# Kernel tuning notes

Measured on AMD Instinct MI355X. Metric: run time of the kernel, lower is better.

Reference implementation:

```python
import jax, jax.numpy as jnp
import numpy as np

N_USER = 100000
N_ITEM = 200000
N_NODES = N_USER + N_ITEM
NNZ = 4000000
EMB = 64
N_LAYERS = 3
BATCH = 4096


def setup_inputs() -> dict:
    key = jax.random.key(0)
    ks = jax.random.split(key, 12)
    inp = {
        'users': jax.random.randint(ks[0], (BATCH,), 0, N_USER, dtype=jnp.int32),
        'pos_items': jax.random.randint(ks[1], (BATCH,), 0, N_ITEM, dtype=jnp.int32),
        'neg_items': jax.random.randint(ks[2], (BATCH,), 0, N_ITEM, dtype=jnp.int32),
        'row': jax.random.randint(ks[3], (NNZ,), 0, N_NODES, dtype=jnp.int32),
        'col': jax.random.randint(ks[4], (NNZ,), 0, N_NODES, dtype=jnp.int32),
        'vals': jax.random.uniform(ks[5], (NNZ,), dtype=jnp.float32),
        'user_emb': 0.1 * jax.random.normal(ks[6], (N_USER, EMB), dtype=jnp.float32),
        'item_emb': 0.1 * jax.random.normal(ks[7], (N_ITEM, EMB), dtype=jnp.float32),
        'W_gc': 0.1 * jax.random.normal(ks[8], (N_LAYERS, EMB, EMB), dtype=jnp.float32),
        'b_gc': 0.1 * jax.random.normal(ks[9], (N_LAYERS, EMB), dtype=jnp.float32),
        'W_bi': 0.1 * jax.random.normal(ks[10], (N_LAYERS, EMB, EMB), dtype=jnp.float32),
        'b_bi': 0.1 * jax.random.normal(ks[11], (N_LAYERS, EMB), dtype=jnp.float32),
    }
    return inp


def _l2_normalize(x, eps=1e-12):
    # matches torch F.normalize(p=2, dim=1): x / max(||x||, eps)
    n = jnp.sqrt(jnp.sum(x * x, axis=1, keepdims=True))
    return x / jnp.maximum(n, eps)


def reference(users, pos_items, neg_items, row, col, vals, user_emb, item_emb, W_gc, b_gc, W_bi, b_bi):
    B = users.shape[0]
    # sparse adjacency propagation: side = A_hat @ [user_emb; item_emb]
    emb = jnp.concatenate([user_emb, item_emb], axis=0)          # [N, d]
    msgs = vals[:, None] * emb[col]                               # [nnz, d]
    side = jax.ops.segment_sum(msgs, row, num_segments=N_NODES)  # [N, d]

    u_side = side[users]                                          # [B, d]
    i_side = jnp.concatenate([side[N_USER + pos_items], side[N_USER + neg_items]], axis=0)
    small_side = jnp.concatenate([u_side, i_side], axis=0)        # [3B, d]
    ego = jnp.concatenate([user_emb[users], item_emb[pos_items], item_emb[neg_items]], axis=0)

    all_embeddings = [ego]
    for k in range(N_LAYERS):
        sum_e = small_side @ W_gc[k] + b_gc[k]
        bi = (ego * small_side) @ W_bi[k] + b_bi[k]
        ego = jax.nn.leaky_relu(sum_e + bi, negative_slope=0.2)
        all_embeddings.append(_l2_normalize(ego))

    all_e = jnp.concatenate(all_embeddings, axis=1)               # [3B, d*(L+1)]
    u_g = all_e[:B]
    i_g = all_e[B:]
    pos_g = i_g[:B]
    neg_g = i_g[B:]
    return (u_g, pos_g, neg_g)
```

## Files before the change

### kernel.cpp

```cpp
#include <hip/hip_runtime.h>

#define N_USER   100000
#define N_ITEM   200000
#define N_NODES  300000
#define NNZ      4000000
#define EMB      64
#define N_LAYERS 3
#define BATCH    4096
#define NSLOT    (3*BATCH)
#define MAXE     96
#define HCAP     256
#define BMWORDS  9376


#define CNT4   3072
#define BM4    2344

__global__ void __launch_bounds__(256) k_clear(int4* __restrict__ c4,
                                               int4* __restrict__ b4) {
    int i = blockIdx.x * blockDim.x + threadIdx.x;
    if (i < CNT4)            c4[i] = make_int4(0, 0, 0, 0);
    else if (i < CNT4 + BM4) b4[i - CNT4] = make_int4(0, 0, 0, 0);
}

__global__ void k_setup(const int* __restrict__ users,
                        const int* __restrict__ pos,
                        const int* __restrict__ neg,
                        unsigned short* __restrict__ table16,
                        unsigned int* __restrict__ bitmap) {
    int i = blockIdx.x * blockDim.x + threadIdx.x;
    if (i >= NSLOT) return;
    int node;
    if (i < BATCH)            node = users[i];
    else if (i < 2 * BATCH)   node = N_USER + pos[i - BATCH];
    else                      node = N_USER + neg[i - 2 * BATCH];
    table16[node] = (unsigned short)i;
    atomicOr(&bitmap[((unsigned)node) >> 5], 1u << (node & 31));
}

__global__ void __launch_bounds__(256) k_build(
        const int* __restrict__ row,
        const int* __restrict__ col,
        const float* __restrict__ vals,
        const unsigned int* __restrict__ bitmap,
        const unsigned short* __restrict__ table16,
        int* __restrict__ count,
        int2* __restrict__ csr2) {
    __shared__ int   ls_s[HCAP];
    __shared__ int   ls_c[HCAP];
    __shared__ float ls_v[HCAP];
    __shared__ int   cnt;
    int tid = threadIdx.x;
    if (tid == 0) cnt = 0;
    __syncthreads();

    int t = blockIdx.x * 256 + tid;
    if (t < NNZ / 4) {
        int4   r = ((const int4*)row)[t];
        int4   c = ((const int4*)col)[t];
        float4 v = ((const float4*)vals)[t];
        bool h0 = (bitmap[((unsigned)r.x) >> 5] >> (r.x & 31)) & 1;
        bool h1 = (bitmap[((unsigned)r.y) >> 5] >> (r.y & 31)) & 1;
        bool h2 = (bitmap[((unsigned)r.z) >> 5] >> (r.z & 31)) & 1;
        bool h3 = (bitmap[((unsigned)r.w) >> 5] >> (r.w & 31)) & 1;
        int rr[4] = { r.x, r.y, r.z, r.w };
        int cc[4] = { c.x, c.y, c.z, c.w };
        float vv[4] = { v.x, v.y, v.z, v.w };
        bool hh[4] = { h0, h1, h2, h3 };
        #pragma unroll
        for (int i = 0; i < 4; ++i) {
            if (hh[i]) {
                int si = (int)table16[rr[i]];
                int p = atomicAdd(&cnt, 1);
                if (p < HCAP) { ls_s[p] = si; ls_c[p] = cc[i]; ls_v[p] = vv[i]; }
                else {
                    int pp = atomicAdd(&count[si], 1);
                    if (pp < MAXE)
                        csr2[(size_t)si * MAXE + pp] = make_int2(cc[i], __float_as_int(vv[i]));
                }
            }
        }
    }
    __syncthreads();

    int n = cnt; n = (n < HCAP) ? n : HCAP;
    for (int t2 = tid; t2 < n; t2 += 256) {
        int si = ls_s[t2];
        int p = atomicAdd(&count[si], 1);
        if (p < MAXE)
            csr2[(size_t)si * MAXE + p] = make_int2(ls_c[t2], __float_as_int(ls_v[t2]));
    }
}

__global__ void __launch_bounds__(256) k_gather(
        const int* __restrict__ users,
        const int* __restrict__ pos,
        const int* __restrict__ neg,
        const float* __restrict__ user_emb,
        const float* __restrict__ item_emb,
        const unsigned short* __restrict__ table16,
        const int* __restrict__ count,
        const int2* __restrict__ csr2,
        float* __restrict__ side) {
    int tid = threadIdx.x;
    int w = tid >> 6;
    int j = tid & 63;
    int slot = blockIdx.x * 4 + w;

    int node;
    if (slot < BATCH)          node = users[slot];
    else if (slot < 2 * BATCH) node = N_USER + pos[slot - BATCH];
    else                       node = N_USER + neg[slot - 2 * BATCH];

    int wslot = (int)table16[node];
    wslot = __builtin_amdgcn_readfirstlane(wslot);
    int n = count[wslot];
    n = (n < MAXE) ? n : MAXE;
    n = __builtin_amdgcn_readfirstlane(n);
    const int2* base = csr2 + (size_t)wslot * MAXE;

    float acc = 0.f;
    for (int t0 = 0; t0 < n; t0 += 64) {
        int idx = t0 + j;
        int2 ev = make_int2(0, 0);
        if (idx < n) ev = base[idx];
        int m = n - t0; m = (m < 64) ? m : 64;
        for (int tt = 0; tt < m; tt += 16) {
            float vv[16], gg[16];
            #pragma unroll
            for (int k = 0; k < 16; ++k) {
                int  t  = tt + k;
                bool okk = t < m;
                int   cc = __shfl(ev.x, t, 64);
                float vb = __uint_as_float((unsigned)__shfl(ev.y, t, 64));
                vv[k] = okk ? vb : 0.f;
                int ci = okk ? cc : 0;
                const float* sp = (ci < N_USER) ? (user_emb + (size_t)ci * EMB)
                                                : (item_emb + (size_t)(ci - N_USER) * EMB);
                gg[k] = sp[j];
            }
            #pragma unroll
            for (int k = 0; k < 16; ++k) acc = fmaf(vv[k], gg[k], acc);
        }
    }
    side[(size_t)slot * EMB + j] = acc;
}

__global__ void __launch_bounds__(256) k_mlp(
        const int* __restrict__ users,
        const int* __restrict__ pos,
        const int* __restrict__ neg,
        const float* __restrict__ user_emb,
        const float* __restrict__ item_emb,
        const float* __restrict__ W_gc,
        const float* __restrict__ b_gc,
        const float* __restrict__ W_bi,
        const float* __restrict__ b_bi,
        const float* __restrict__ side,
        float* __restrict__ out) {
    __shared__ float wg[EMB * EMB];
    __shared__ float wb[EMB * EMB];
    int tid = threadIdx.x;
    int w = tid >> 6;
    int j = tid & 63;
    int sbase = blockIdx.x * 16 + w * 4;

    float sval[4], e[4];
    #pragma unroll
    for (int s = 0; s < 4; ++s) {
        int slot = sbase + s;
        int node;
        if (slot < BATCH)          node = users[slot];
        else if (slot < 2 * BATCH) node = N_USER + pos[slot - BATCH];
        else                       node = N_USER + neg[slot - 2 * BATCH];
        const float* erow = (node < N_USER) ? (user_emb + (size_t)node * EMB)
                                            : (item_emb + (size_t)(node - N_USER) * EMB);
        e[s]    = erow[j];
        sval[s] = side[(size_t)slot * EMB + j];
        out[(size_t)slot * 256 + j] = e[s];
    }

    for (int k = 0; k < N_LAYERS; ++k) {
        __syncthreads();
        {
            const float4* g4 = (const float4*)(W_gc + (size_t)k * EMB * EMB);
            const float4* b4 = (const float4*)(W_bi + (size_t)k * EMB * EMB);
            float4* lg = (float4*)wg;
            float4* lb = (float4*)wb;
            #pragma unroll
            for (int i2 = tid; i2 < EMB * EMB / 4; i2 += 256) { lg[i2] = g4[i2]; lb[i2] = b4[i2]; }
        }
        __syncthreads();

        float b1 = b_gc[k * EMB + j];
        float b2 = b_bi[k * EMB + j];
        float sum1[4], sum2[4], pv[4];
        #pragma unroll
        for (int s = 0; s < 4; ++s) { sum1[s] = b1; sum2[s] = b2; pv[s] = sval[s] * e[s]; }

        #pragma unroll 8
        for (int i = 0; i < EMB; ++i) {
            float wgi = wg[i * EMB + j];
            float wbi = wb[i * EMB + j];
            #pragma unroll
            for (int s = 0; s < 4; ++s) {
                float si = __uint_as_float(__builtin_amdgcn_readlane(__float_as_uint(sval[s]), i));
                float pi = __uint_as_float(__builtin_amdgcn_readlane(__float_as_uint(pv[s]),   i));
                sum1[s] = fmaf(si, wgi, sum1[s]);
                sum2[s] = fmaf(pi, wbi, sum2[s]);
            }
        }

        #pragma unroll
        for (int s = 0; s < 4; ++s) {
            float x = sum1[s] + sum2[s];
            x = (x >= 0.f) ? x : 0.2f * x;
            float sq = x * x;
            #pragma unroll
            for (int o = 32; o; o >>= 1) sq += __shfl_xor(sq, o, 64);
            float nn = fmaxf(sqrtf(sq), 1e-12f);
            out[(size_t)(sbase + s) * 256 + (k + 1) * 64 + j] = x / nn;
            e[s] = x;
        }
    }
}

extern "C" void kernel_launch(void* const* d_in, const int* in_sizes, int n_in,
                              void* d_out, int out_size, void* d_ws, size_t ws_size,
                              hipStream_t stream) {
    const int*   users    = (const int*)  d_in[0];
    const int*   pos      = (const int*)  d_in[1];
    const int*   neg      = (const int*)  d_in[2];
    const int*   row      = (const int*)  d_in[3];
    const int*   col      = (const int*)  d_in[4];
    const float* vals     = (const float*)d_in[5];
    const float* user_emb = (const float*)d_in[6];
    const float* item_emb = (const float*)d_in[7];
    const float* W_gc     = (const float*)d_in[8];
    const float* b_gc     = (const float*)d_in[9];
    const float* W_bi     = (const float*)d_in[10];
    const float* b_bi     = (const float*)d_in[11];
    float* out = (float*)d_out;

    char* ws = (char*)d_ws;
    unsigned short* table16 = (unsigned short*)ws;
    int*            count   = (int*)(ws + 600064);
    int2*           csr2    = (int2*)(ws + 649216);
    float*          side    = (float*)(ws + 10086400);
    unsigned int*   bitmap  = (unsigned int*)(ws + 13232128);

    k_clear<<<(CNT4 + BM4 + 255) / 256, 256, 0, stream>>>((int4*)count, (int4*)bitmap);
    k_setup<<<(NSLOT + 255) / 256, 256, 0, stream>>>(users, pos, neg, table16, bitmap);
    k_build<<<(NNZ / 4 + 255) / 256, 256, 0, stream>>>(row, col, vals, bitmap,
                                                       table16, count, csr2);
    k_gather<<<NSLOT / 4, 256, 0, stream>>>(users, pos, neg, user_emb, item_emb,
                                            table16, count, csr2, side);
    k_mlp<<<NSLOT / 16, 256, 0, stream>>>(users, pos, neg, user_emb, item_emb,
                                          W_gc, b_gc, W_bi, b_bi, side, out);
}
```

Measured before the change: 76.79 us.

## Fold count clearing into setup, double build work per block, simplify gather and mlp

Clearing of the count array moves from the clear kernel into the setup kernel, and the workspace is reordered so the bitmap sits before side. Each build block now processes two int4 chunks, so half as many blocks launch. The gather kernel loads the first 64 edges once and handles any overflow serially, removing the outer loop. The mlp kernel drops the shared-memory staging of the weights and reads them directly from global/L1 with half the slots per block, which removes the barriers but repeats weight reads from cache.

Result: no change. 77.51 us (+0.9%).

```diff
diff --git a/kernel.cpp b/kernel.cpp
--- a/kernel.cpp
+++ b/kernel.cpp
@@ -13,23 +13,22 @@
 #define BMWORDS  9376
 
 
-#define CNT4   3072
 #define BM4    2344
 
-__global__ void __launch_bounds__(256) k_clear(int4* __restrict__ c4,
-                                               int4* __restrict__ b4) {
+__global__ void __launch_bounds__(256) k_clear(int4* __restrict__ b4) {
     int i = blockIdx.x * blockDim.x + threadIdx.x;
-    if (i < CNT4)            c4[i] = make_int4(0, 0, 0, 0);
-    else if (i < CNT4 + BM4) b4[i - CNT4] = make_int4(0, 0, 0, 0);
+    if (i < BM4) b4[i] = make_int4(0, 0, 0, 0);
 }
 
 __global__ void k_setup(const int* __restrict__ users,
                         const int* __restrict__ pos,
                         const int* __restrict__ neg,
                         unsigned short* __restrict__ table16,
-                        unsigned int* __restrict__ bitmap) {
+                        unsigned int* __restrict__ bitmap,
+                        int* __restrict__ count) {
     int i = blockIdx.x * blockDim.x + threadIdx.x;
     if (i >= NSLOT) return;
+    count[i] = 0;
     int node;
     if (i < BATCH)            node = users[i];
     else if (i < 2 * BATCH)   node = N_USER + pos[i - BATCH];
@@ -54,29 +53,33 @@
     if (tid == 0) cnt = 0;
     __syncthreads();
 
-    int t = blockIdx.x * 256 + tid;
-    if (t < NNZ / 4) {
-        int4   r = ((const int4*)row)[t];
-        int4   c = ((const int4*)col)[t];
-        float4 v = ((const float4*)vals)[t];
-        bool h0 = (bitmap[((unsigned)r.x) >> 5] >> (r.x & 31)) & 1;
-        bool h1 = (bitmap[((unsigned)r.y) >> 5] >> (r.y & 31)) & 1;
-        bool h2 = (bitmap[((unsigned)r.z) >> 5] >> (r.z & 31)) & 1;
-        bool h3 = (bitmap[((unsigned)r.w) >> 5] >> (r.w & 31)) & 1;
-        int rr[4] = { r.x, r.y, r.z, r.w };
-        int cc[4] = { c.x, c.y, c.z, c.w };
-        float vv[4] = { v.x, v.y, v.z, v.w };
-        bool hh[4] = { h0, h1, h2, h3 };
-        #pragma unroll
-        for (int i = 0; i < 4; ++i) {
-            if (hh[i]) {
-                int si = (int)table16[rr[i]];
-                int p = atomicAdd(&cnt, 1);
-                if (p < HCAP) { ls_s[p] = si; ls_c[p] = cc[i]; ls_v[p] = vv[i]; }
-                else {
-                    int pp = atomicAdd(&count[si], 1);
-                    if (pp < MAXE)
-                        csr2[(size_t)si * MAXE + pp] = make_int2(cc[i], __float_as_int(vv[i]));
+    const int nt4 = NNZ / 4;
+    #pragma unroll
+    for (int q = 0; q < 2; ++q) {
+        int t = blockIdx.x * 512 + q * 256 + tid;
+        if (t < nt4) {
+            int4   r = ((const int4*)row)[t];
+            int4   c = ((const int4*)col)[t];
+            float4 v = ((const float4*)vals)[t];
+            bool h0 = (bitmap[((unsigned)r.x) >> 5] >> (r.x & 31)) & 1;
+            bool h1 = (bitmap[((unsigned)r.y) >> 5] >> (r.y & 31)) & 1;
+            bool h2 = (bitmap[((unsigned)r.z) >> 5] >> (r.z & 31)) & 1;
+            bool h3 = (bitmap[((unsigned)r.w) >> 5] >> (r.w & 31)) & 1;
+            int rr[4] = { r.x, r.y, r.z, r.w };
+            int cc[4] = { c.x, c.y, c.z, c.w };
+            float vv[4] = { v.x, v.y, v.z, v.w };
+            bool hh[4] = { h0, h1, h2, h3 };
+            #pragma unroll
+            for (int i = 0; i < 4; ++i) {
+                if (hh[i]) {
+                    int si = (int)table16[rr[i]];
+                    int p = atomicAdd(&cnt, 1);
+                    if (p < HCAP) { ls_s[p] = si; ls_c[p] = cc[i]; ls_v[p] = vv[i]; }
+                    else {
+                        int pp = atomicAdd(&count[si], 1);
+                        if (pp < MAXE)
+                            csr2[(size_t)si * MAXE + pp] = make_int2(cc[i], __float_as_int(vv[i]));
+                    }
                 }
             }
         }
@@ -119,29 +122,33 @@
     n = __builtin_amdgcn_readfirstlane(n);
     const int2* base = csr2 + (size_t)wslot * MAXE;
 
+    int2 ev = make_int2(0, 0);
+    if (j < n) ev = base[j];
+
     float acc = 0.f;
-    for (int t0 = 0; t0 < n; t0 += 64) {
-        int idx = t0 + j;
-        int2 ev = make_int2(0, 0);
-        if (idx < n) ev = base[idx];
-        int m = n - t0; m = (m < 64) ? m : 64;
-        for (int tt = 0; tt < m; tt += 16) {
-            float vv[16], gg[16];
-            #pragma unroll
-            for (int k = 0; k < 16; ++k) {
-                int  t  = tt + k;
-                bool okk = t < m;
-                int   cc = __shfl(ev.x, t, 64);
-                float vb = __uint_as_float((unsigned)__shfl(ev.y, t, 64));
-                vv[k] = okk ? vb : 0.f;
-                int ci = okk ? cc : 0;
-                const float* sp = (ci < N_USER) ? (user_emb + (size_t)ci * EMB)
-                                                : (item_emb + (size_t)(ci - N_USER) * EMB);
-                gg[k] = sp[j];
-            }
-            #pragma unroll
-            for (int k = 0; k < 16; ++k) acc = fmaf(vv[k], gg[k], acc);
-        }
+    int m = (n < 64) ? n : 64;
+    for (int tt = 0; tt < m; tt += 16) {
+        float vv[16], gg[16];
+        #pragma unroll
+        for (int k = 0; k < 16; ++k) {
+            int  t  = tt + k;
+            bool okk = t < m;
+            int   cc = __shfl(ev.x, t, 64);
+            float vb = __uint_as_float((unsigned)__shfl(ev.y, t, 64));
+            vv[k] = okk ? vb : 0.f;
+            int ci = okk ? cc : 0;
+            const float* sp = (ci < N_USER) ? (user_emb + (size_t)ci * EMB)
+                                            : (item_emb + (size_t)(ci - N_USER) * EMB);
+            gg[k] = sp[j];
+        }
+        #pragma unroll
+        for (int k = 0; k < 16; ++k) acc = fmaf(vv[k], gg[k], acc);
+    }
+    for (int t = 64; t < n; ++t) {
+        int2 ee = base[t];
+        const float* sp = (ee.x < N_USER) ? (user_emb + (size_t)ee.x * EMB)
+                                          : (item_emb + (size_t)(ee.x - N_USER) * EMB);
+        acc = fmaf(__uint_as_float((unsigned)ee.y), sp[j], acc);
     }
     side[(size_t)slot * EMB + j] = acc;
 }
@@ -158,16 +165,14 @@
         const float* __restrict__ b_bi,
         const float* __restrict__ side,
         float* __restrict__ out) {
-    __shared__ float wg[EMB * EMB];
-    __shared__ float wb[EMB * EMB];
     int tid = threadIdx.x;
     int w = tid >> 6;
     int j = tid & 63;
-    int sbase = blockIdx.x * 16 + w * 4;
-
-    float sval[4], e[4];
+    int sbase = blockIdx.x * 8 + w * 2;
+
+    float sval[2], e[2];
     #pragma unroll
-    for (int s = 0; s < 4; ++s) {
+    for (int s = 0; s < 2; ++s) {
         int slot = sbase + s;
         int node;
         if (slot < BATCH)          node = users[slot];
@@ -181,29 +186,20 @@
     }
 
     for (int k = 0; k < N_LAYERS; ++k) {
-        __syncthreads();
-        {
-            const float4* g4 = (const float4*)(W_gc + (size_t)k * EMB * EMB);
-            const float4* b4 = (const float4*)(W_bi + (size_t)k * EMB * EMB);
-            float4* lg = (float4*)wg;
-            float4* lb = (float4*)wb;
-            #pragma unroll
-            for (int i2 = tid; i2 < EMB * EMB / 4; i2 += 256) { lg[i2] = g4[i2]; lb[i2] = b4[i2]; }
-        }
-        __syncthreads();
-
+        const float* wg = W_gc + (size_t)k * EMB * EMB;
+        const float* wb = W_bi + (size_t)k * EMB * EMB;
         float b1 = b_gc[k * EMB + j];
         float b2 = b_bi[k * EMB + j];
-        float sum1[4], sum2[4], pv[4];
-        #pragma unroll
-        for (int s = 0; s < 4; ++s) { sum1[s] = b1; sum2[s] = b2; pv[s] = sval[s] * e[s]; }
+        float sum1[2], sum2[2], pv[2];
+        #pragma unroll
+        for (int s = 0; s < 2; ++s) { sum1[s] = b1; sum2[s] = b2; pv[s] = sval[s] * e[s]; }
 
         #pragma unroll 8
         for (int i = 0; i < EMB; ++i) {
             float wgi = wg[i * EMB + j];
             float wbi = wb[i * EMB + j];
             #pragma unroll
-            for (int s = 0; s < 4; ++s) {
+            for (int s = 0; s < 2; ++s) {
                 float si = __uint_as_float(__builtin_amdgcn_readlane(__float_as_uint(sval[s]), i));
                 float pi = __uint_as_float(__builtin_amdgcn_readlane(__float_as_uint(pv[s]),   i));
                 sum1[s] = fmaf(si, wgi, sum1[s]);
@@ -212,7 +208,7 @@
         }
 
         #pragma unroll
-        for (int s = 0; s < 4; ++s) {
+        for (int s = 0; s < 2; ++s) {
             float x = sum1[s] + sum2[s];
             x = (x >= 0.f) ? x : 0.2f * x;
             float sq = x * x;
@@ -246,15 +242,16 @@
     unsigned short* table16 = (unsigned short*)ws;
     int*            count   = (int*)(ws + 600064);
     int2*           csr2    = (int2*)(ws + 649216);
-    float*          side    = (float*)(ws + 10086400);
-    unsigned int*   bitmap  = (unsigned int*)(ws + 13232128);
-
-    k_clear<<<(CNT4 + BM4 + 255) / 256, 256, 0, stream>>>((int4*)count, (int4*)bitmap);
-    k_setup<<<(NSLOT + 255) / 256, 256, 0, stream>>>(users, pos, neg, table16, bitmap);
-    k_build<<<(NNZ / 4 + 255) / 256, 256, 0, stream>>>(row, col, vals, bitmap,
+    unsigned int*   bitmap  = (unsigned int*)(ws + 10086400);
+    float*          side    = (float*)(ws + 10124032);
+
+    k_clear<<<(BM4 + 255) / 256, 256, 0, stream>>>((int4*)bitmap);
+    k_setup<<<(NSLOT + 255) / 256, 256, 0, stream>>>(users, pos, neg, table16,
+                                                     bitmap, count);
+    k_build<<<(NNZ / 4 + 511) / 512, 256, 0, stream>>>(row, col, vals, bitmap,
                                                        table16, count, csr2);
     k_gather<<<NSLOT / 4, 256, 0, stream>>>(users, pos, neg, user_emb, item_emb,
                                             table16, count, csr2, side);
-    k_mlp<<<NSLOT / 16, 256, 0, stream>>>(users, pos, neg, user_emb, item_emb,
-                                          W_gc, b_gc, W_bi, b_bi, side, out);
-}
+    k_mlp<<<NSLOT / 8, 256, 0, stream>>>(users, pos, neg, user_emb, item_emb,
+                                         W_gc, b_gc, W_bi, b_bi, side, out);
+}
```
